# Kernel tuning notes

Hardware: AMD Instinct MI355X
Metric: run time of the kernel (lower is better)

## Reference

```python
import jax, jax.numpy as jnp
from jax import lax
import numpy as np

DIM, HEADS, WIN = 192, 8, 8
B, H, W = 4, 256, 256


def setup_inputs() -> dict:
    key = jax.random.key(0)
    ks = jax.random.split(key, 4)
    s = 0.02
    return {
        "x": jax.random.normal(ks[0], (B, DIM, H, W), jnp.float32),
        "temperature": jnp.ones((HEADS, 1, 1), jnp.float32),
        "qkv_w": jax.random.normal(ks[1], (3 * DIM, DIM, 1, 1), jnp.float32) * s,
        "qkv_b": jnp.zeros((3 * DIM,), jnp.float32),
        "dw_w": jax.random.normal(ks[2], (3 * DIM, 1, 3, 3), jnp.float32) * s,
        "dw_b": jnp.zeros((3 * DIM,), jnp.float32),
        "proj_w": jax.random.normal(ks[3], (DIM, DIM, 1, 1), jnp.float32) * s,
        "proj_b": jnp.zeros((DIM,), jnp.float32),
    }


def _conv(x, w, b, groups=1, pad='VALID'):
    y = lax.conv_general_dilated(x, w, (1, 1), pad,
                                 feature_group_count=groups,
                                 dimension_numbers=('NCHW', 'OIHW', 'NCHW'))
    return y + b[None, :, None, None]


def _l2norm(x, eps=1e-12):
    # F.normalize(dim=-1): x / max(||x||_2, eps)
    n = jnp.sqrt(jnp.sum(x * x, axis=-1, keepdims=True))
    return x / jnp.maximum(n, eps)


def _chan_attn(q, k, v, temp):
    # q,k,v: [n, heads, c_per_head, d]; channel-wise (CxC) attention
    q = _l2norm(q)
    k = _l2norm(k)
    attn = jnp.einsum('nhcd,nhed->nhce', q, k) * temp[None]
    attn = jax.nn.softmax(attn, axis=-1)
    return jnp.einsum('nhce,nhed->nhcd', attn, v)


def reference(x, temperature, qkv_w, qkv_b, dw_w, dw_b, proj_w, proj_b):
    b, c, h, w = x.shape
    win, heads = WIN, HEADS
    cph = c // heads

    qkv = _conv(x, qkv_w, qkv_b)
    qkv = _conv(qkv, dw_w, dw_b, groups=3 * c, pad='SAME')  # depthwise 3x3
    q, k, v = jnp.split(qkv, 3, axis=1)

    # ---- local (windowed) branch ----
    def win_part(t):
        t = t.reshape(b, c, h // win, win, w // win, win)
        t = t.transpose(0, 2, 4, 1, 3, 5)
        return t.reshape(-1, heads, cph, win * win)

    o1 = _chan_attn(win_part(q), win_part(k), win_part(v), temperature)
    o1 = o1.reshape(b, h // win, w // win, c, win, win)
    o1 = o1.transpose(0, 3, 1, 4, 2, 5).reshape(b, c, h, w)

    # ---- global branch ----
    def flat(t):
        return t.reshape(b, heads, cph, h * w)

    o2 = _chan_attn(flat(q), flat(k), flat(v), temperature)
    o2 = o2.reshape(b, c, h, w)

    return _conv(o1 + o2, proj_w, proj_b)
```

## Files before the change

### kernel.cpp

```cpp
#include <hip/hip_runtime.h>
#include <hip/hip_bf16.h>
#include <cstdint>
#include <cstddef>

#define HWPIX 65536
#define IMGW 256
#define CDIM 192
#define C3 576
#define NBATCH 4
#define NHEADS 8
#define CPH 24
#define KP 104

using bf16 = __hip_bfloat16;
typedef __attribute__((ext_vector_type(8))) short short8;
typedef __attribute__((ext_vector_type(4))) float f32x4;
typedef unsigned int u32;
typedef unsigned short u16;

__device__ __forceinline__ float b2f(bf16 v) { return __bfloat162float(v); }
__device__ __forceinline__ bf16 f2b(float v) { return __float2bfloat16(v); }
__device__ __forceinline__ float bu2f(u16 h) { return __uint_as_float((u32)h << 16); }
__device__ __forceinline__ u16 f2bu(float x) {
    bf16 h = __float2bfloat16(x);
    return *reinterpret_cast<u16*>(&h);
}
__device__ __forceinline__ u32 pack2(float a, float b) {
    return (u32)f2bu(a) | ((u32)f2bu(b) << 16);
}

__global__ __launch_bounds__(256) void prep_weights(
    const float* __restrict__ W, u16* __restrict__ Wb, int n)
{
    int i = blockIdx.x * 256 + threadIdx.x;
    if (i < n) Wb[i] = f2bu(W[i]);
}

__global__ __launch_bounds__(256) void xprep_kernel(
    const float* __restrict__ X, u16* __restrict__ Xt)
{
    __shared__ float sX[CDIM * 68];
    const int b  = blockIdx.y;
    const int p0 = blockIdx.x * 64;
    const int tid = threadIdx.x;

#pragma unroll
    for (int i = 0; i < 12; ++i) {
        const int idx = tid + i * 256;
        const int p4 = idx & 15, k = idx >> 4;
        const float4 v = *reinterpret_cast<const float4*>(
            X + ((size_t)b * CDIM + k) * HWPIX + p0 + p4 * 4);
        *reinterpret_cast<float4*>(&sX[k * 68 + p4 * 4]) = v;
    }
    __syncthreads();

    const int p = tid >> 2;
    const int seg = tid & 3;
    u16* dst = Xt + ((size_t)b * HWPIX + p0 + p) * CDIM;
#pragma unroll
    for (int s = 0; s < 6; ++s) {
        const int blk = seg * 6 + s;
        float f[8];
#pragma unroll
        for (int j = 0; j < 8; ++j) f[j] = sX[(blk * 8 + j) * 68 + p];
        uint4 ov;
        ov.x = pack2(f[0], f[1]);
        ov.y = pack2(f[2], f[3]);
        ov.z = pack2(f[4], f[5]);
        ov.w = pack2(f[6], f[7]);
        *reinterpret_cast<uint4*>(dst + blk * 8) = ov;
    }
}

__device__ __forceinline__ void chunk_mfma(
    const u16* sA, const u16* sB, int r, int hk, int wave, f32x4 (&acc)[4][2])
{
#pragma unroll
    for (int ks = 0; ks < 3; ++ks) {
        const int kof = ks * 32 + hk * 8;
        const u16* pA = &sA[r * KP + kof];
        const u16* pB = &sB[(wave * 32 + r) * KP + kof];
        const short8 a0 = *reinterpret_cast<const short8*>(pA);
        const short8 a1 = *reinterpret_cast<const short8*>(pA + 16 * KP);
        const short8 a2 = *reinterpret_cast<const short8*>(pA + 32 * KP);
        const short8 a3 = *reinterpret_cast<const short8*>(pA + 48 * KP);
        const short8 b0 = *reinterpret_cast<const short8*>(pB);
        const short8 b1 = *reinterpret_cast<const short8*>(pB + 16 * KP);
        acc[0][0] = __builtin_amdgcn_mfma_f32_16x16x32_bf16(a0, b0, acc[0][0], 0, 0, 0);
        acc[1][0] = __builtin_amdgcn_mfma_f32_16x16x32_bf16(a1, b0, acc[1][0], 0, 0, 0);
        acc[2][0] = __builtin_amdgcn_mfma_f32_16x16x32_bf16(a2, b0, acc[2][0], 0, 0, 0);
        acc[3][0] = __builtin_amdgcn_mfma_f32_16x16x32_bf16(a3, b0, acc[3][0], 0, 0, 0);
        acc[0][1] = __builtin_amdgcn_mfma_f32_16x16x32_bf16(a0, b1, acc[0][1], 0, 0, 0);
        acc[1][1] = __builtin_amdgcn_mfma_f32_16x16x32_bf16(a1, b1, acc[1][1], 0, 0, 0);
        acc[2][1] = __builtin_amdgcn_mfma_f32_16x16x32_bf16(a2, b1, acc[2][1], 0, 0, 0);
        acc[3][1] = __builtin_amdgcn_mfma_f32_16x16x32_bf16(a3, b1, acc[3][1], 0, 0, 0);
    }
}

__global__ __launch_bounds__(256, 4) void conv_qkv_mfma(
    const u16* __restrict__ Xt, const u16* __restrict__ Wb,
    const float* __restrict__ bias, bf16* __restrict__ Y)
{
    __shared__ alignas(16) u16 sA[64 * KP];
    __shared__ alignas(16) u16 sB[128 * KP];
    __shared__ float sBias[64];

    int lin = blockIdx.x;
    lin = (lin & 7) * (18432 / 8) + (lin >> 3);
    const int co_t = lin % 9;
    const int rest = lin / 9;
    const int p_t = rest & 511;
    const int b   = rest >> 9;
    const int co0 = co_t * 64;
    const int p0  = p_t * 128;

    const int tid  = threadIdx.x;
    const int wave = tid >> 6;
    const int lane = tid & 63;
    const int r  = lane & 15;
    const int hk = lane >> 4;

    if (tid < 64) sBias[tid] = bias[co0 + tid];

    f32x4 acc[4][2];
#pragma unroll
    for (int i = 0; i < 4; ++i)
#pragma unroll
        for (int j = 0; j < 2; ++j) acc[i][j] = (f32x4){0.f, 0.f, 0.f, 0.f};

#pragma unroll
    for (int c = 0; c < 2; ++c) {
        {
            int idx = tid;
#pragma unroll
            for (int i = 0; i < 3; ++i, idx += 256) {
                const int row = idx / 12, cv = idx % 12;
                const uint4 v = *reinterpret_cast<const uint4*>(
                    Wb + (size_t)(co0 + row) * CDIM + c * 96 + cv * 8);
                *reinterpret_cast<uint4*>(&sA[row * KP + cv * 8]) = v;
            }
        }
        {
            int idx = tid;
#pragma unroll
            for (int i = 0; i < 6; ++i, idx += 256) {
                const int row = idx / 12, cv = idx % 12;
                const uint4 v = *reinterpret_cast<const uint4*>(
                    Xt + ((size_t)b * HWPIX + p0 + row) * CDIM + c * 96 + cv * 8);
                *reinterpret_cast<uint4*>(&sB[row * KP + cv * 8]) = v;
            }
        }
        __syncthreads();
        chunk_mfma(sA, sB, r, hk, wave, acc);
        __syncthreads();
    }

#define OS2 132
    u16* sOut = sB;
#pragma unroll
    for (int mf = 0; mf < 4; ++mf) {
#pragma unroll
        for (int j = 0; j < 4; ++j) {
            const int row = mf * 16 + hk * 4 + j;
            const float bs = sBias[row];
            sOut[row * OS2 + wave * 32 + r]      = f2bu(acc[mf][0][j] + bs);
            sOut[row * OS2 + wave * 32 + r + 16] = f2bu(acc[mf][1][j] + bs);
        }
    }
    __syncthreads();
#pragma unroll
    for (int i = 0; i < 4; ++i) {
        const int idx = tid + i * 256;
        const int row = idx >> 4, cq = idx & 15;
        const u16* src = &sOut[row * OS2 + cq * 8];
        const uint2 lo = *reinterpret_cast<const uint2*>(src);
        const uint2 hi = *reinterpret_cast<const uint2*>(src + 4);
        uint4 v = {lo.x, lo.y, hi.x, hi.y};
        *reinterpret_cast<uint4*>(
            &Y[((size_t)b * C3 + co0 + row) * HWPIX + p0 + cq * 8]) = v;
    }
}

__global__ __launch_bounds__(256, 4) void conv_proj_mfma(
    const u16* __restrict__ Ot, const u16* __restrict__ Wb,
    const float* __restrict__ bias, float* __restrict__ Y)
{
    __shared__ alignas(16) u16 sA[64 * KP];
    __shared__ alignas(16) u16 sB[128 * KP];
    __shared__ float sBias[64];

    int lin = blockIdx.x;
    lin = (lin & 7) * (6144 / 8) + (lin >> 3);
    const int co_t = lin % 3;
    const int rest = lin / 3;
    const int p_t = rest & 511;
    const int b   = rest >> 9;
    const int co0 = co_t * 64;
    const int p0  = p_t * 128;

    const int tid  = threadIdx.x;
    const int wave = tid >> 6;
    const int lane = tid & 63;
    const int r  = lane & 15;
    const int hk = lane >> 4;

    if (tid < 64) sBias[tid] = bias[co0 + tid];

    f32x4 acc[4][2];
#pragma unroll
    for (int i = 0; i < 4; ++i)
#pragma unroll
        for (int j = 0; j < 2; ++j) acc[i][j] = (f32x4){0.f, 0.f, 0.f, 0.f};

#pragma unroll
    for (int c = 0; c < 2; ++c) {
        {
            int idx = tid;
#pragma unroll
            for (int i = 0; i < 3; ++i, idx += 256) {
                const int row = idx / 12, cv = idx % 12;
                const uint4 v = *reinterpret_cast<const uint4*>(
                    Wb + (size_t)(co0 + row) * CDIM + c * 96 + cv * 8);
                *reinterpret_cast<uint4*>(&sA[row * KP + cv * 8]) = v;
            }
        }
        {
            int idx = tid;
#pragma unroll
            for (int i = 0; i < 6; ++i, idx += 256) {
                const int row = idx / 12, sub = idx % 12;
                const int h = c * 4 + sub / 3, part = sub % 3;
                const uint4 v = *reinterpret_cast<const uint4*>(
                    Ot + ((size_t)(b * NHEADS + h) * HWPIX + p0 + row) * CPH + part * 8);
                *reinterpret_cast<uint4*>(
                    &sB[row * KP + (sub / 3) * 24 + part * 8]) = v;
            }
        }
        __syncthreads();
        chunk_mfma(sA, sB, r, hk, wave, acc);
        __syncthreads();
    }

#pragma unroll
    for (int mf = 0; mf < 4; ++mf) {
#pragma unroll
        for (int j = 0; j < 4; ++j) {
            const int co = co0 + mf * 16 + hk * 4 + j;
            const float bs = sBias[mf * 16 + hk * 4 + j];
            const size_t base = ((size_t)b * CDIM + co) * HWPIX + p0 + wave * 32 + r;
            Y[base]      = acc[mf][0][j] + bs;
            Y[base + 16] = acc[mf][1][j] + bs;
        }
    }
}

__global__ __launch_bounds__(256) void dwconv_kernel(
    const bf16* __restrict__ In, const float* __restrict__ Wd,
    const float* __restrict__ bd, bf16* __restrict__ Out)
{
    __shared__ alignas(16) u16 sIn[34 * 256];
    const int bc = blockIdx.y;
    const int c = bc % C3;
    const size_t base = (size_t)bc * HWPIX;
    const int r0 = blockIdx.x * 32;
    const int tid = threadIdx.x;

    for (int idx = tid; idx < 34 * 32; idx += 256) {
        const int lr = idx >> 5, ch = idx & 31;
        const int gr = r0 + lr - 1;
        uint4 v = {0u, 0u, 0u, 0u};
        if ((unsigned)gr < IMGW)
            v = *reinterpret_cast<const uint4*>(&In[base + (size_t)gr * IMGW + ch * 8]);
        *reinterpret_cast<uint4*>(&sIn[lr * 256 + ch * 8]) = v;
    }
    __syncthreads();

    float wg[9];
#pragma unroll
    for (int t = 0; t < 9; ++t) wg[t] = Wd[c * 9 + t];

    const int rr  = tid >> 5;
    const int px0 = (tid & 31) * 8;
    const float bias = bd[c];

#pragma unroll
    for (int kk = 0; kk < 4; ++kk) {
        const int orow = rr + kk * 8;
        float acc[8];
#pragma unroll
        for (int j = 0; j < 8; ++j) acc[j] = bias;

#pragma unroll
        for (int dy = 0; dy < 3; ++dy) {
            const u16* rp = &sIn[(orow + dy) * 256];
            const short8 mv = *reinterpret_cast<const short8*>(&rp[px0]);
            float m[8];
#pragma unroll
            for (int j = 0; j < 8; ++j) m[j] = bu2f((u16)mv[j]);
            const float lft = (px0 > 0) ? bu2f(rp[px0 - 1]) : 0.f;
            const float rgt = (px0 + 8 < 256) ? bu2f(rp[px0 + 8]) : 0.f;
            const float w0 = wg[dy * 3], w1 = wg[dy * 3 + 1], w2 = wg[dy * 3 + 2];

            acc[0] = fmaf(w0, lft, acc[0]);
            acc[0] = fmaf(w1, m[0], acc[0]);
            acc[0] = fmaf(w2, m[1], acc[0]);
#pragma unroll
            for (int j = 1; j < 7; ++j) {
                acc[j] = fmaf(w0, m[j - 1], acc[j]);
                acc[j] = fmaf(w1, m[j], acc[j]);
                acc[j] = fmaf(w2, m[j + 1], acc[j]);
            }
            acc[7] = fmaf(w0, m[6], acc[7]);
            acc[7] = fmaf(w1, m[7], acc[7]);
            acc[7] = fmaf(w2, rgt, acc[7]);
        }

        uint4 ov;
        ov.x = pack2(acc[0], acc[1]);
        ov.y = pack2(acc[2], acc[3]);
        ov.z = pack2(acc[4], acc[5]);
        ov.w = pack2(acc[6], acc[7]);
        *reinterpret_cast<uint4*>(&Out[base + (size_t)(r0 + orow) * IMGW + px0]) = ov;
    }
}

#define CS 328
#define PS 40
#define OS3 28

__global__ __launch_bounds__(256, 3) void local_attn_kernel(
    const bf16* __restrict__ QKV, const float* __restrict__ temp,
    const float* __restrict__ Ag, u16* __restrict__ Ot)
{
    __shared__ alignas(16) u16 sMem[3 * 24 * CS];
    __shared__ float snq[4 * 32], snk[4 * 32];
    __shared__ float sAg[576];
    u16* const sQ = sMem;
    u16* const sK = sMem + 24 * CS;
    u16* const sV = sMem + 48 * CS;
    u16* const sP = sQ;
    u16* const sO = sK;

    const int wy    = blockIdx.x >> 3;
    const int strip = blockIdx.x & 7;
    const int head  = blockIdx.y;
    const int b     = blockIdx.z;
    const int x0    = strip * 32;
    const int tid   = threadIdx.x;
    const int w     = tid >> 6;
    const int lane  = tid & 63;
    const int r     = lane & 15;
    const int hk    = lane >> 4;

    {
        const float* Asrc = Ag + ((size_t)(b * NHEADS + head)) * 576;
        for (int idx = tid; idx < 576; idx += 256) sAg[idx] = Asrc[idx];
    }

#pragma unroll
    for (int i = 0; i < 9; ++i) {
        const int idx = tid + i * 256;
        const int tensor = idx / 768;
        const int rem = idx - tensor * 768;
        const int c  = rem >> 5;
        const int rw = (rem >> 2) & 7;
        const int ch = rem & 3;
        const size_t g = ((size_t)b * C3 + tensor * CDIM + head * CPH + c) * HWPIX
                       + (size_t)(wy * 8 + rw) * IMGW + x0 + ch * 8;
        const uint4 v = *reinterpret_cast<const uint4*>(&QKV[g]);
        u16* dst = sMem + tensor * (24 * CS);
        *reinterpret_cast<uint4*>(&dst[c * CS + rw * 40 + ch * 8]) = v;
    }
    __syncthreads();

    if (tid < 192) {
        const int qk = tid / 96;
        const int rem = tid - qk * 96;
        const int ww = rem / 24, c = rem % 24;
        const u16* sT = qk ? sK : sQ;
        const int off = c * CS + ww * 8;
        float s = 0.f;
#pragma unroll
        for (int rw = 0; rw < 8; ++rw) {
            const int rw2 = (rw + c) & 7;
            const short8 v = *reinterpret_cast<const short8*>(&sT[off + rw2 * 40]);
#pragma unroll
            for (int j = 0; j < 8; ++j) {
                const float f = bu2f((u16)v[j]);
                s = fmaf(f, f, s);
            }
        }
        const float inv = 1.f / fmaxf(sqrtf(s), 1e-12f);
        if (qk) snk[ww * 32 + c] = inv; else snq[ww * 32 + c] = inv;
    }
    __syncthreads();

    f32x4 accg[2][2];
#pragma unroll
    for (int i = 0; i < 2; ++i)
#pragma unroll
        for (int j = 0; j < 2; ++j) accg[i][j] = (f32x4){0.f, 0.f, 0.f, 0.f};

    __builtin_amdgcn_s_setprio(1);
#pragma unroll
    for (int kk = 0; kk < 2; ++kk) {
        const int colA = (kk * 4 + hk) * 40 + w * 8;
        const short8 aq0 = *reinterpret_cast<const short8*>(&sQ[(r     ) * CS + colA]);
        const short8 aq1 = *reinterpret_cast<const short8*>(&sQ[(16 + r) * CS + colA]);
        const short8 bk0 = *reinterpret_cast<const short8*>(&sK[(r     ) * CS + colA]);
        const short8 bk1 = *reinterpret_cast<const short8*>(&sK[(16 + r) * CS + colA]);
        accg[0][0] = __builtin_amdgcn_mfma_f32_16x16x32_bf16(aq0, bk0, accg[0][0], 0, 0, 0);
        accg[0][1] = __builtin_amdgcn_mfma_f32_16x16x32_bf16(aq0, bk1, accg[0][1], 0, 0, 0);
        accg[1][0] = __builtin_amdgcn_mfma_f32_16x16x32_bf16(aq1, bk0, accg[1][0], 0, 0, 0);
        accg[1][1] = __builtin_amdgcn_mfma_f32_16x16x32_bf16(aq1, bk1, accg[1][1], 0, 0, 0);
    }
    __builtin_amdgcn_s_setprio(0);
    __syncthreads();

    const float t = temp[head];
    const int e0 = lane & 15;
    const bool v1 = e0 < 8;
    const float ink0 = snk[w * 32 + e0];
    const float ink1 = snk[w * 32 + 16 + e0];

#pragma unroll
    for (int ct = 0; ct < 2; ++ct) {
#pragma unroll
        for (int j = 0; j < 4; ++j) {
            const int cidx = ct * 16 + hk * 4 + j;
            const float inq = snq[w * 32 + (cidx < CPH ? cidx : 0)];
            const float g0 = accg[ct][0][j] * inq * ink0 * t;
            const float g1 = v1 ? accg[ct][1][j] * inq * ink1 * t : -1e30f;
            float m = fmaxf(g0, g1);
#pragma unroll
            for (int mk = 8; mk >= 1; mk >>= 1) m = fmaxf(m, __shfl_xor(m, mk));
            const float p0 = __expf(g0 - m);
            const float p1 = v1 ? __expf(g1 - m) : 0.f;
            float s = p0 + p1;
#pragma unroll
            for (int mk = 8; mk >= 1; mk >>= 1) s += __shfl_xor(s, mk);
            const float inv = 1.f / s;
            if (cidx < CPH) {
                sP[w * 32 * PS + cidx * PS + e0] = f2bu(p0 * inv + sAg[cidx * CPH + e0]);
                if (v1) sP[w * 32 * PS + cidx * PS + 16 + e0]
                    = f2bu(p1 * inv + sAg[cidx * CPH + 16 + e0]);
            }
        }
    }
    __syncthreads();

    f32x4 acco[2][4];
#pragma unroll
    for (int i = 0; i < 2; ++i)
#pragma unroll
        for (int j = 0; j < 4; ++j) acco[i][j] = (f32x4){0.f, 0.f, 0.f, 0.f};

    short8 afr[2];
#pragma unroll
    for (int ct = 0; ct < 2; ++ct) {
        if (hk < 3)
            afr[ct] = *reinterpret_cast<const short8*>(
                &sP[w * 32 * PS + (ct * 16 + r) * PS + hk * 8]);
        else
            afr[ct] = (short8){0, 0, 0, 0, 0, 0, 0, 0};
    }
    __builtin_amdgcn_s_setprio(1);
#pragma unroll
    for (int nt = 0; nt < 4; ++nt) {
        const int px = nt * 16 + r;
        const int colV = (px >> 3) * 40 + w * 8 + (px & 7);
        short8 bfr;
        if (hk < 3) {
#pragma unroll
            for (int j = 0; j < 8; ++j)
                bfr[j] = (short)sV[(hk * 8 + j) * CS + colV];
        } else {
            bfr = (short8){0, 0, 0, 0, 0, 0, 0, 0};
        }
        acco[0][nt] = __builtin_amdgcn_mfma_f32_16x16x32_bf16(afr[0], bfr, acco[0][nt], 0, 0, 0);
        acco[1][nt] = __builtin_amdgcn_mfma_f32_16x16x32_bf16(afr[1], bfr, acco[1][nt], 0, 0, 0);
    }
    __builtin_amdgcn_s_setprio(0);

#pragma unroll
    for (int ct = 0; ct < 2; ++ct) {
#pragma unroll
        for (int j = 0; j < 4; ++j) {
            const int cidx = ct * 16 + hk * 4 + j;
            if (cidx >= CPH) continue;
#pragma unroll
            for (int nt = 0; nt < 4; ++nt) {
                const int px = nt * 16 + r;
                const int rpx = px >> 3, pxl = px & 7;
                const int lp = rpx * 32 + w * 8 + pxl;
                sO[lp * OS3 + cidx] = f2bu(acco[ct][nt][j]);
            }
        }
    }
    __syncthreads();

    {
        const int lp = tid;
        const int gp = (wy * 8 + (lp >> 5)) * IMGW + x0 + (lp & 31);
        const u16* src = &sO[lp * OS3];
        uint2 d0 = *reinterpret_cast<const uint2*>(src);
        uint2 d1 = *reinterpret_cast<const uint2*>(src + 4);
        uint2 d2 = *reinterpret_cast<const uint2*>(src + 8);
        uint2 d3 = *reinterpret_cast<const uint2*>(src + 12);
        uint2 d4 = *reinterpret_cast<const uint2*>(src + 16);
        uint2 d5 = *reinterpret_cast<const uint2*>(src + 20);
        u16* dst = Ot + ((size_t)(b * NHEADS + head) * HWPIX + gp) * CPH;
        uint4 v0 = {d0.x, d0.y, d1.x, d1.y};
        uint4 v1 = {d2.x, d2.y, d3.x, d3.y};
        uint4 v2 = {d4.x, d4.y, d5.x, d5.y};
        *reinterpret_cast<uint4*>(dst)      = v0;
        *reinterpret_cast<uint4*>(dst + 8)  = v1;
        *reinterpret_cast<uint4*>(dst + 16) = v2;
    }
}

#define GRS 520

__global__ __launch_bounds__(256) void gstats_kernel(
    const bf16* __restrict__ QKV, float* __restrict__ Gp)
{
    __shared__ alignas(16) u16 sq[32 * GRS];
    __shared__ alignas(16) u16 sk[32 * GRS];

    const int chunk = blockIdx.x;
    const int bh = blockIdx.y;
    const int b = bh >> 3, head = bh & 7;
    const int tid = threadIdx.x;
    const int w = tid >> 6, lane = tid & 63;
    const int r = lane & 15, hk = lane >> 4;

    const size_t qb = ((size_t)b * C3 + head * CPH) * HWPIX;
    const size_t kb = qb + (size_t)CDIM * HWPIX;

    for (int idx = tid; idx < 1040; idx += 256) {
        const int t = idx >= 520;
        const int o = idx - t * 520;
        u16* d = (t ? sk : sq) + 24 * GRS + o * 8;
        *reinterpret_cast<uint4*>(d) = (uint4){0u, 0u, 0u, 0u};
    }

    f32x4 acc[2][2];
#pragma unroll
    for (int i = 0; i < 2; ++i)
#pragma unroll
        for (int j = 0; j < 2; ++j) acc[i][j] = (f32x4){0.f, 0.f, 0.f, 0.f};
    float nacc = 0.f;
    const int nrow = tid >> 2;
    const int nq4  = tid & 3;

    for (int st = 0; st < 8; ++st) {
        const int d0 = chunk * 4096 + st * 512;
        __syncthreads();
#pragma unroll
        for (int i = 0; i < 12; ++i) {
            const int idx = tid + i * 256;
            const int t = idx >= 1536;
            const int rem = idx - t * 1536;
            const int c = rem >> 6, dv = rem & 63;
            const uint4 v = *reinterpret_cast<const uint4*>(
                &QKV[(t ? kb : qb) + (size_t)c * HWPIX + d0 + dv * 8]);
            u16* dst = (t ? sk : sq) + c * GRS + dv * 8;
            *reinterpret_cast<uint4*>(dst) = v;
        }
        __syncthreads();

#pragma unroll
        for (int ks = 0; ks < 4; ++ks) {
            const int kof = w * 128 + ks * 32 + hk * 8;
            const short8 aq0 = *reinterpret_cast<const short8*>(&sq[(r     ) * GRS + kof]);
            const short8 aq1 = *reinterpret_cast<const short8*>(&sq[(16 + r) * GRS + kof]);
            const short8 bk0 = *reinterpret_cast<const short8*>(&sk[(r     ) * GRS + kof]);
            const short8 bk1 = *reinterpret_cast<const short8*>(&sk[(16 + r) * GRS + kof]);
            acc[0][0] = __builtin_amdgcn_mfma_f32_16x16x32_bf16(aq0, bk0, acc[0][0], 0, 0, 0);
            acc[0][1] = __builtin_amdgcn_mfma_f32_16x16x32_bf16(aq0, bk1, acc[0][1], 0, 0, 0);
            acc[1][0] = __builtin_amdgcn_mfma_f32_16x16x32_bf16(aq1, bk0, acc[1][0], 0, 0, 0);
            acc[1][1] = __builtin_amdgcn_mfma_f32_16x16x32_bf16(aq1, bk1, acc[1][1], 0, 0, 0);
        }

        if (nrow < 48) {
            const u16* rp = (nrow < 24 ? &sq[nrow * GRS] : &sk[(nrow - 24) * GRS]) + nq4 * 128;
#pragma unroll
            for (int i = 0; i < 16; ++i) {
                const short8 v = *reinterpret_cast<const short8*>(&rp[i * 8]);
#pragma unroll
                for (int j = 0; j < 8; ++j) {
                    const float f = bu2f((u16)v[j]);
                    nacc = fmaf(f, f, nacc);
                }
            }
        }
    }
    __syncthreads();

    float* red = reinterpret_cast<float*>(sq);
#pragma unroll
    for (int ct = 0; ct < 2; ++ct) {
#pragma unroll
        for (int et = 0; et < 2; ++et) {
#pragma unroll
            for (int j = 0; j < 4; ++j) {
                const int c = ct * 16 + hk * 4 + j;
                const int e = et * 16 + r;
                if (c < CPH && e < CPH)
                    red[(w * 24 + c) * 25 + e] = acc[ct][et][j];
            }
        }
    }
    __syncthreads();

    float* dst = Gp + ((size_t)bh * 32 + chunk) * 624;
    for (int idx = tid; idx < 576; idx += 256) {
        const int c = idx / 24, e = idx % 24;
        const int o = c * 25 + e;
        dst[idx] = red[o] + red[600 + o] + red[1200 + o] + red[1800 + o];
    }

    float ns = nacc;
    ns += __shfl_xor(ns, 1);
    ns += __shfl_xor(ns, 2);
    if (nrow < 48 && nq4 == 0) {
        if (nrow < 24) dst[576 + nrow] = ns;
        else           dst[600 + (nrow - 24)] = ns;
    }
}

__global__ __launch_bounds__(64) void gsoftmax_kernel(
    const float* __restrict__ Gp, const float* __restrict__ temp,
    float* __restrict__ A)
{
    __shared__ float red[624];
    const int bh = blockIdx.x, head = bh & 7;
    const int tid = threadIdx.x;

    for (int jj = tid; jj < 624; jj += 64) {
        float s = 0.f;
        for (int ch = 0; ch < 16; ++ch) s += Gp[((size_t)bh * 32 + ch) * 624 + jj];
        red[jj] = s;
    }
    __syncthreads();

    if (tid < CPH) {
        const int c = tid;
        const float t = temp[head];
        const float inq = 1.f / fmaxf(sqrtf(red[576 + c]), 1e-12f);
        float l[CPH]; float m = -1e30f;
        for (int e = 0; e < CPH; ++e) {
            const float ink = 1.f / fmaxf(sqrtf(red[600 + e]), 1e-12f);
            l[e] = red[c * CPH + e] * inq * ink * t;
            m = fmaxf(m, l[e]);
        }
        float s = 0.f;
        for (int e = 0; e < CPH; ++e) { l[e] = expf(l[e] - m); s += l[e]; }
        const float inv = 1.f / s;
        for (int e = 0; e < CPH; ++e) A[(size_t)bh * 576 + c * CPH + e] = l[e] * inv;
    }
}

extern "C" void kernel_launch(void* const* d_in, const int* in_sizes, int n_in,
                              void* d_out, int out_size, void* d_ws, size_t ws_size,
                              hipStream_t stream) {
    const float* x           = (const float*)d_in[0];
    const float* temperature = (const float*)d_in[1];
    const float* qkv_w       = (const float*)d_in[2];
    const float* qkv_b       = (const float*)d_in[3];
    const float* dw_w        = (const float*)d_in[4];
    const float* dw_b        = (const float*)d_in[5];
    const float* proj_w      = (const float*)d_in[6];
    const float* proj_b      = (const float*)d_in[7];
    float* out = (float*)d_out;

    char* ws = (char*)d_ws;
    constexpr size_t QKV_ELEMS = (size_t)NBATCH * C3 * HWPIX;
    constexpr size_t QKV_BYTES = QKV_ELEMS * sizeof(bf16);

    bf16* qkv1 = (bf16*)ws;
    bf16* qkv2 = (bf16*)(ws + QKV_BYTES);
    u16*  osumT = (u16*)ws;
    float* Gp   = (float*)(ws + 2 * QKV_BYTES);
    float* Amat = Gp + (size_t)32 * 32 * 624;
    u16*  Wb    = (u16*)Gp;
    u16*  Wpb   = (u16*)(Amat + 32 * 576);
    u16*  Xt    = (u16*)qkv2;

    prep_weights<<<(C3 * CDIM + 255) / 256, 256, 0, stream>>>(qkv_w, Wb, C3 * CDIM);
    prep_weights<<<(CDIM * CDIM + 255) / 256, 256, 0, stream>>>(proj_w, Wpb, CDIM * CDIM);

    xprep_kernel<<<dim3(HWPIX / 64, NBATCH), 256, 0, stream>>>(x, Xt);

    conv_qkv_mfma<<<9 * 512 * NBATCH, 256, 0, stream>>>(Xt, Wb, qkv_b, qkv1);

    dwconv_kernel<<<dim3(8, NBATCH * C3), 256, 0, stream>>>(
        qkv1, dw_w, dw_b, qkv2);

    gstats_kernel<<<dim3(16, 32), 256, 0, stream>>>(qkv2, Gp);

    gsoftmax_kernel<<<32, 64, 0, stream>>>(Gp, temperature, Amat);

    local_attn_kernel<<<dim3(256, NHEADS, NBATCH), 256, 0, stream>>>(
        qkv2, temperature, Amat, osumT);

    conv_proj_mfma<<<3 * 512 * NBATCH, 256, 0, stream>>>(osumT, Wpb, proj_b, out);
}
```

Measured before the change: 607.7 us.

## Shrink local attention LDS by deferring V load into Q buffer; merge weight prep

The local attention kernel now allocates shared memory for only Q and K. V is loaded into registers from global memory while the softmax runs, then written into the Q region after the QK MFMA is done. The launch bound rises to 4 blocks per CU to use the freed LDS. P and O now share the K region, which needs an extra barrier, and holding V in registers raises register pressure. The two weight-conversion launches are also merged into one kernel.

Measured after the change: 594.0 us (median of 2 runs). -2.3%, faster.

```diff
diff --git a/kernel.cpp b/kernel.cpp
--- a/kernel.cpp
+++ b/kernel.cpp
@@ -29,11 +29,13 @@
     return (u32)f2bu(a) | ((u32)f2bu(b) << 16);
 }
 
-__global__ __launch_bounds__(256) void prep_weights(
-    const float* __restrict__ W, u16* __restrict__ Wb, int n)
+__global__ __launch_bounds__(256) void prep_weights2(
+    const float* __restrict__ W1, u16* __restrict__ O1, int n1,
+    const float* __restrict__ W2, u16* __restrict__ O2, int n2)
 {
     int i = blockIdx.x * 256 + threadIdx.x;
-    if (i < n) Wb[i] = f2bu(W[i]);
+    if (i < n1) O1[i] = f2bu(W1[i]);
+    else if (i < n1 + n2) O2[i - n1] = f2bu(W2[i - n1]);
 }
 
 __global__ __launch_bounds__(256) void xprep_kernel(
@@ -328,18 +330,18 @@
 #define PS 40
 #define OS3 28
 
-__global__ __launch_bounds__(256, 3) void local_attn_kernel(
+__global__ __launch_bounds__(256, 4) void local_attn_kernel(
     const bf16* __restrict__ QKV, const float* __restrict__ temp,
     const float* __restrict__ Ag, u16* __restrict__ Ot)
 {
-    __shared__ alignas(16) u16 sMem[3 * 24 * CS];
+    __shared__ alignas(16) u16 sMem[2 * 24 * CS];
     __shared__ float snq[4 * 32], snk[4 * 32];
     __shared__ float sAg[576];
     u16* const sQ = sMem;
     u16* const sK = sMem + 24 * CS;
-    u16* const sV = sMem + 48 * CS;
-    u16* const sP = sQ;
-    u16* const sO = sK;
+    u16* const sV = sMem;
+    u16* const sP = sMem + 24 * CS;
+    u16* const sO = sMem + 24 * CS;
 
     const int wy    = blockIdx.x >> 3;
     const int strip = blockIdx.x & 7;
@@ -358,7 +360,7 @@
     }
 
 #pragma unroll
-    for (int i = 0; i < 9; ++i) {
+    for (int i = 0; i < 6; ++i) {
         const int idx = tid + i * 256;
         const int tensor = idx / 768;
         const int rem = idx - tensor * 768;
@@ -417,6 +419,29 @@
     __builtin_amdgcn_s_setprio(0);
     __syncthreads();
 
+    uint4 vr0, vr1, vr2;
+    int vl0, vl1, vl2;
+    {
+        const int idx0 = tid;
+        const int c0 = idx0 >> 5, rw0 = (idx0 >> 2) & 7, ch0 = idx0 & 3;
+        vr0 = *reinterpret_cast<const uint4*>(&QKV[
+            ((size_t)b * C3 + 2 * CDIM + head * CPH + c0) * HWPIX
+            + (size_t)(wy * 8 + rw0) * IMGW + x0 + ch0 * 8]);
+        vl0 = c0 * CS + rw0 * 40 + ch0 * 8;
+        const int idx1 = tid + 256;
+        const int c1 = idx1 >> 5, rw1 = (idx1 >> 2) & 7, ch1 = idx1 & 3;
+        vr1 = *reinterpret_cast<const uint4*>(&QKV[
+            ((size_t)b * C3 + 2 * CDIM + head * CPH + c1) * HWPIX
+            + (size_t)(wy * 8 + rw1) * IMGW + x0 + ch1 * 8]);
+        vl1 = c1 * CS + rw1 * 40 + ch1 * 8;
+        const int idx2 = tid + 512;
+        const int c2 = idx2 >> 5, rw2 = (idx2 >> 2) & 7, ch2 = idx2 & 3;
+        vr2 = *reinterpret_cast<const uint4*>(&QKV[
+            ((size_t)b * C3 + 2 * CDIM + head * CPH + c2) * HWPIX
+            + (size_t)(wy * 8 + rw2) * IMGW + x0 + ch2 * 8]);
+        vl2 = c2 * CS + rw2 * 40 + ch2 * 8;
+    }
+
     const float t = temp[head];
     const int e0 = lane & 15;
     const bool v1 = e0 < 8;
@@ -447,6 +472,10 @@
             }
         }
     }
+
+    *reinterpret_cast<uint4*>(&sV[vl0]) = vr0;
+    *reinterpret_cast<uint4*>(&sV[vl1]) = vr1;
+    *reinterpret_cast<uint4*>(&sV[vl2]) = vr2;
     __syncthreads();
 
     f32x4 acco[2][4];
@@ -481,6 +510,7 @@
         acco[1][nt] = __builtin_amdgcn_mfma_f32_16x16x32_bf16(afr[1], bfr, acco[1][nt], 0, 0, 0);
     }
     __builtin_amdgcn_s_setprio(0);
+    __syncthreads();
 
 #pragma unroll
     for (int ct = 0; ct < 2; ++ct) {
@@ -687,8 +717,8 @@
     u16*  Wpb   = (u16*)(Amat + 32 * 576);
     u16*  Xt    = (u16*)qkv2;
 
-    prep_weights<<<(C3 * CDIM + 255) / 256, 256, 0, stream>>>(qkv_w, Wb, C3 * CDIM);
-    prep_weights<<<(CDIM * CDIM + 255) / 256, 256, 0, stream>>>(proj_w, Wpb, CDIM * CDIM);
+    prep_weights2<<<(C3 * CDIM + CDIM * CDIM + 255) / 256, 256, 0, stream>>>(
+        qkv_w, Wb, C3 * CDIM, proj_w, Wpb, CDIM * CDIM);
 
     xprep_kernel<<<dim3(HWPIX / 64, NBATCH), 256, 0, stream>>>(x, Xt);
 
```
